# Optimization experiments

Measured on AMD Instinct MI355X. Metric: run time of the kernel, lower is better.

The kernel has to match this reference:

```python
import jax, jax.numpy as jnp
import numpy as np

B, C, H, W = 16, 64, 128, 128


def setup_inputs() -> dict:
    key = jax.random.key(0)
    k1, k2, k3 = jax.random.split(key, 3)
    return {
        "template_map": jax.random.normal(k1, (B, C, H, W), dtype=jnp.float32),
        "roi_map": jax.random.normal(k2, (B, C, H, W), dtype=jnp.float32),
        "gamma": jnp.zeros((1,), dtype=jnp.float32),
        "omega": jnp.zeros((1,), dtype=jnp.float32),
        "conv_w": jax.random.normal(k3, (C, 2 * C), dtype=jnp.float32) * 0.05,
        "conv_b": jnp.zeros((C,), dtype=jnp.float32),
    }


def _chan_attn(x):
    # x: [B, C, H, W] -> attention over channels [B, C, C] and flat values [B, C, N]
    b, c, h, w = x.shape
    v = x.reshape(b, c, h * w)
    energy = jnp.einsum('bcn,bdn->bcd', v, v)  # [B, C, C]
    energy_new = jnp.max(energy, axis=-1, keepdims=True) - energy
    attn = jax.nn.softmax(energy_new, axis=-1)
    return attn, v


def reference(template_map, roi_map, gamma, omega, conv_w, conv_b):
    b, c, th, tw = template_map.shape
    _, _, rh, rw = roi_map.shape
    t_attn, t_v = _chan_attn(template_map)
    r_attn, r_v = _chan_attn(roi_map)
    # cross application: roi attention reweights template channels, and vice versa
    t_out = jnp.einsum('bcd,bdn->bcn', r_attn, t_v).reshape(b, c, th, tw)
    t_out = gamma * t_out + template_map
    r_out = jnp.einsum('bcd,bdn->bcn', t_attn, r_v).reshape(b, c, rh, rw)
    r_out = omega * r_out + roi_map
    fused = jnp.concatenate([t_out, r_out], axis=1)  # [B, 2C, H, W]
    # 1x1 conv == channel-mixing einsum
    out = jnp.einsum('bchw,oc->bohw', fused, conv_w) + conv_b[None, :, None, None]
    return out
```

## Files before the change

### kernel.cpp

```cpp
#include <hip/hip_runtime.h>

typedef __attribute__((ext_vector_type(8))) short short8;
typedef __attribute__((ext_vector_type(4))) float floatx4;
typedef unsigned int uint;
typedef unsigned short ushort;

#define BATCH 16
#define CH 64
#define NPIX 16384
#define TWOC 128
#define XSTR 260

__device__ __forceinline__ ushort f2bf(float f) {
    uint u = __float_as_uint(f);
    u += 0x7FFFu + ((u >> 16) & 1u);
    return (ushort)(u >> 16);
}
__device__ __forceinline__ uint pk2(float lo, float hi) {
    return (uint)f2bf(lo) | ((uint)f2bf(hi) << 16);
}

__global__ __launch_bounds__(256) void gram_kernel(
    const float* __restrict__ tmap, const float* __restrict__ rmap,
    const float* __restrict__ gamma, const float* __restrict__ omega,
    float* __restrict__ G)
{
    const int map = blockIdx.y;
    const float mult = (map == 0) ? omega[0] : gamma[0];
    if (mult == 0.f) return;

    __shared__ float tile[64][68];
    const int chunk = blockIdx.x;
    const int b     = blockIdx.z;
    const float* x = (map == 0 ? tmap : rmap) + (size_t)b * CH * NPIX + chunk * 512;
    const int t  = threadIdx.x;
    const int ti = t >> 4;
    const int tj = t & 15;

    float acc[4][4];
#pragma unroll
    for (int i = 0; i < 4; ++i)
#pragma unroll
        for (int j = 0; j < 4; ++j) acc[i][j] = 0.f;

    for (int tt = 0; tt < 8; ++tt) {
        const int col0 = tt * 64;
#pragma unroll
        for (int k = 0; k < 16; ++k) {
            int e = t + 256 * k;
            int c = e >> 6, col = e & 63;
            tile[c][col] = x[(size_t)c * NPIX + col0 + col];
        }
        __syncthreads();
#pragma unroll 8
        for (int n = 0; n < 64; n += 2) {
            float2 av[4], bv[4];
#pragma unroll
            for (int i = 0; i < 4; ++i) av[i] = *(const float2*)&tile[ti + 16 * i][n];
#pragma unroll
            for (int j = 0; j < 4; ++j) bv[j] = *(const float2*)&tile[tj + 16 * j][n];
#pragma unroll
            for (int i = 0; i < 4; ++i)
#pragma unroll
                for (int j = 0; j < 4; ++j) {
                    acc[i][j] += av[i].x * bv[j].x;
                    acc[i][j] += av[i].y * bv[j].y;
                }
        }
        __syncthreads();
    }
    float* Gp = G + ((size_t)(b * 2 + map) << 12);
#pragma unroll
    for (int i = 0; i < 4; ++i)
#pragma unroll
        for (int j = 0; j < 4; ++j)
            atomicAdd(&Gp[(ti + 16 * i) * 64 + (tj + 16 * j)], acc[i][j]);
}

__global__ __launch_bounds__(128) void finalize_kernel(
    const float* __restrict__ G, const float* __restrict__ gamma,
    const float* __restrict__ omega, const float* __restrict__ conv_w,
    ushort* __restrict__ Mtf)
{
    __shared__ float attn[2][64][64];
    const int b = blockIdx.x;
    const int t = threadIdx.x;
    const float gam = gamma[0], om = omega[0];
    {
        const int map = t >> 6, i = t & 63;
        const float need = (map == 0) ? om : gam;
        if (need != 0.f) {
            const float* Grow = G + ((size_t)(b * 2 + map) << 12) + i * 64;
            float mn = Grow[0];
            for (int j = 1; j < 64; ++j) mn = fminf(mn, Grow[j]);
            float s = 0.f;
            for (int j = 0; j < 64; ++j) s += expf(mn - Grow[j]);
            const float inv = 1.f / s;
            for (int j = 0; j < 64; ++j) attn[map][i][j] = expf(mn - Grow[j]) * inv;
        }
    }
    __syncthreads();
    for (int idx = t; idx < 8192; idx += 128) {
        const int e     = idx & 7;
        const int l     = (idx >> 3) & 63;
        const int mi    = (idx >> 9) & 3;
        const int kstep = idx >> 11;
        const int row = mi * 16 + (l & 15);
        const int k   = kstep * 32 + (l >> 4) * 8 + e;
        const float* wrow = conv_w + row * TWOC;
        float v = wrow[k];
        if (k < 64) {
            if (gam != 0.f) {
                float dot = 0.f;
                for (int c = 0; c < 64; ++c) dot += wrow[c] * attn[1][c][k];
                v += gam * dot;
            }
        } else {
            const int d = k - 64;
            if (om != 0.f) {
                float dot = 0.f;
                for (int c = 0; c < 64; ++c) dot += wrow[64 + c] * attn[0][c][d];
                v += om * dot;
            }
        }
        Mtf[(size_t)b * 8192 + idx] = f2bf(v);
    }
}

__global__ __launch_bounds__(256, 4) void out_kernel(
    const float* __restrict__ tmap, const float* __restrict__ rmap,
    const ushort* __restrict__ Mtf, const float* __restrict__ conv_b,
    float* __restrict__ out)
{
    __shared__ __align__(16) ushort Ms[8192];
    __shared__ __align__(16) uint   Xs[16 * XSTR];

    const int b   = blockIdx.y;
    const int t   = threadIdx.x;
    const int w   = t >> 6;
    const int l   = t & 63;
    const int lg  = l >> 4;
    const int lj  = l & 15;
    const int px0 = blockIdx.x * 256;

    {
        const uint4* src = (const uint4*)(Mtf + (size_t)b * 8192);
        uint4* dst = (uint4*)Ms;
#pragma unroll
        for (int i = 0; i < 4; ++i) dst[t + 256 * i] = src[t + 256 * i];
    }

    floatx4 acc[4][4];
#pragma unroll
    for (int mi = 0; mi < 4; ++mi)
#pragma unroll
        for (int nj = 0; nj < 4; ++nj) acc[mi][nj] = (floatx4){0.f, 0.f, 0.f, 0.f};

    const float* tb = tmap + (size_t)b * CH * NPIX + px0;
    const float* rb = rmap + (size_t)b * CH * NPIX + px0;

#pragma unroll
    for (int c = 0; c < 4; ++c) {
        const float* src = ((c < 2) ? tb : rb) + (size_t)((c & 1) * 32) * NPIX;

        float4 r0[4], r1[4];
#pragma unroll
        for (int it = 0; it < 4; ++it) {
            const int p = it * 4 + w;
            r0[it] = *(const float4*)&src[(size_t)(2 * p) * NPIX + 4 * l];
            r1[it] = *(const float4*)&src[(size_t)(2 * p + 1) * NPIX + 4 * l];
        }
        __syncthreads();

#pragma unroll
        for (int it = 0; it < 4; ++it) {
            const int p = it * 4 + w;
            uint4 o;
            o.x = pk2(r0[it].x, r1[it].x);
            o.y = pk2(r0[it].y, r1[it].y);
            o.z = pk2(r0[it].z, r1[it].z);
            o.w = pk2(r0[it].w, r1[it].w);
            *(uint4*)&Xs[p * XSTR + 4 * l] = o;
        }
        __syncthreads();

        short8 a[4];
#pragma unroll
        for (int mi = 0; mi < 4; ++mi)
            a[mi] = *(const short8*)&Ms[((c * 4 + mi) * 64 + l) * 8];

#pragma unroll
        for (int nj = 0; nj < 4; ++nj) {
            const int pxl = w * 64 + nj * 16 + lj;
            uint4 bu;
            bu.x = Xs[(4 * lg + 0) * XSTR + pxl];
            bu.y = Xs[(4 * lg + 1) * XSTR + pxl];
            bu.z = Xs[(4 * lg + 2) * XSTR + pxl];
            bu.w = Xs[(4 * lg + 3) * XSTR + pxl];
            const short8 bb = *(const short8*)&bu;
#pragma unroll
            for (int mi = 0; mi < 4; ++mi)
                acc[mi][nj] = __builtin_amdgcn_mfma_f32_16x16x32_bf16(
                    a[mi], bb, acc[mi][nj], 0, 0, 0);
        }
    }

    const int pxw = px0 + w * 64;
#pragma unroll
    for (int mi = 0; mi < 4; ++mi) {
#pragma unroll
        for (int r = 0; r < 4; ++r) {
            const int och = mi * 16 + lg * 4 + r;
            const float bv = conv_b[och];
            float* orow = out + ((size_t)b * CH + och) * NPIX;
#pragma unroll
            for (int nj = 0; nj < 4; ++nj)
                orow[pxw + nj * 16 + lj] = acc[mi][nj][r] + bv;
        }
    }
}

extern "C" void kernel_launch(void* const* d_in, const int* in_sizes, int n_in,
                              void* d_out, int out_size, void* d_ws, size_t ws_size,
                              hipStream_t stream) {
    const float* tmap   = (const float*)d_in[0];
    const float* rmap   = (const float*)d_in[1];
    const float* gamma  = (const float*)d_in[2];
    const float* omega  = (const float*)d_in[3];
    const float* conv_w = (const float*)d_in[4];
    const float* conv_b = (const float*)d_in[5];
    float* out = (float*)d_out;

    float*  G   = (float*)d_ws;
    ushort* Mtf = (ushort*)((char*)d_ws + (size_t)BATCH * 2 * 4096 * sizeof(float));

    hipMemsetAsync(d_ws, 0, (size_t)BATCH * 2 * 4096 * sizeof(float), stream);

    gram_kernel<<<dim3(32, 2, BATCH), 256, 0, stream>>>(tmap, rmap, gamma, omega, G);
    finalize_kernel<<<dim3(BATCH), 128, 0, stream>>>(G, gamma, omega, conv_w, Mtf);
    out_kernel<<<dim3(64, BATCH), 256, 0, stream>>>(tmap, rmap, Mtf, conv_b, out);
}
```

Before: 54.46 us.

## Shrink out_kernel to single-wave blocks, drop barriers and LDS weight staging

Restructures the output GEMM kernel so each block is one 64-lane wave handling 64 pixels, with 4x as many blocks. Because a single wave owns its LDS tile, the __syncthreads barriers become an explicit lgkmcnt wait, and the bf16 weight matrix is read straight from global memory/cache instead of being staged in shared memory. This removes barrier stalls and LDS staging overhead and raises the number of independent waves available to hide latency. In exchange, each wave re-reads the weight fragments from global memory, and the smaller per-block pixel span yields shorter 256-byte contiguous row segments per load.

```diff
diff --git a/kernel.cpp b/kernel.cpp
--- a/kernel.cpp
+++ b/kernel.cpp
@@ -9,7 +9,7 @@
 #define CH 64
 #define NPIX 16384
 #define TWOC 128
-#define XSTR 260
+#define XSTR 68
 
 __device__ __forceinline__ ushort f2bf(float f) {
     uint u = __float_as_uint(f);
@@ -127,37 +127,28 @@
     }
 }
 
-__global__ __launch_bounds__(256, 4) void out_kernel(
+__global__ __launch_bounds__(64, 4) void out_kernel(
     const float* __restrict__ tmap, const float* __restrict__ rmap,
     const ushort* __restrict__ Mtf, const float* __restrict__ conv_b,
     float* __restrict__ out)
 {
-    __shared__ __align__(16) ushort Ms[8192];
-    __shared__ __align__(16) uint   Xs[16 * XSTR];
+    __shared__ __align__(16) uint Xs[16 * XSTR];
 
     const int b   = blockIdx.y;
-    const int t   = threadIdx.x;
-    const int w   = t >> 6;
-    const int l   = t & 63;
+    const int l   = threadIdx.x;
     const int lg  = l >> 4;
     const int lj  = l & 15;
-    const int px0 = blockIdx.x * 256;
-
-    {
-        const uint4* src = (const uint4*)(Mtf + (size_t)b * 8192);
-        uint4* dst = (uint4*)Ms;
-#pragma unroll
-        for (int i = 0; i < 4; ++i) dst[t + 256 * i] = src[t + 256 * i];
-    }
+    const int pxw = blockIdx.x * 64;
+
+    const ushort* mbase = Mtf + (size_t)b * 8192;
+    const float*  tb = tmap + (size_t)b * CH * NPIX + pxw;
+    const float*  rb = rmap + (size_t)b * CH * NPIX + pxw;
 
     floatx4 acc[4][4];
 #pragma unroll
     for (int mi = 0; mi < 4; ++mi)
 #pragma unroll
         for (int nj = 0; nj < 4; ++nj) acc[mi][nj] = (floatx4){0.f, 0.f, 0.f, 0.f};
-
-    const float* tb = tmap + (size_t)b * CH * NPIX + px0;
-    const float* rb = rmap + (size_t)b * CH * NPIX + px0;
 
 #pragma unroll
     for (int c = 0; c < 4; ++c) {
@@ -166,37 +157,37 @@
         float4 r0[4], r1[4];
 #pragma unroll
         for (int it = 0; it < 4; ++it) {
-            const int p = it * 4 + w;
-            r0[it] = *(const float4*)&src[(size_t)(2 * p) * NPIX + 4 * l];
-            r1[it] = *(const float4*)&src[(size_t)(2 * p + 1) * NPIX + 4 * l];
-        }
-        __syncthreads();
+            const int p = it * 4 + lg;
+            r0[it] = *(const float4*)&src[(size_t)(2 * p) * NPIX + 4 * lj];
+            r1[it] = *(const float4*)&src[(size_t)(2 * p + 1) * NPIX + 4 * lj];
+        }
 
 #pragma unroll
         for (int it = 0; it < 4; ++it) {
-            const int p = it * 4 + w;
+            const int p = it * 4 + lg;
             uint4 o;
             o.x = pk2(r0[it].x, r1[it].x);
             o.y = pk2(r0[it].y, r1[it].y);
             o.z = pk2(r0[it].z, r1[it].z);
             o.w = pk2(r0[it].w, r1[it].w);
-            *(uint4*)&Xs[p * XSTR + 4 * l] = o;
-        }
-        __syncthreads();
+            *(uint4*)&Xs[p * XSTR + 4 * lj] = o;
+        }
 
         short8 a[4];
 #pragma unroll
         for (int mi = 0; mi < 4; ++mi)
-            a[mi] = *(const short8*)&Ms[((c * 4 + mi) * 64 + l) * 8];
+            a[mi] = *(const short8*)&mbase[((c * 4 + mi) * 64 + l) * 8];
+
+        asm volatile("s_waitcnt lgkmcnt(0)" ::: "memory");
+        __builtin_amdgcn_sched_barrier(0);
 
 #pragma unroll
         for (int nj = 0; nj < 4; ++nj) {
-            const int pxl = w * 64 + nj * 16 + lj;
             uint4 bu;
-            bu.x = Xs[(4 * lg + 0) * XSTR + pxl];
-            bu.y = Xs[(4 * lg + 1) * XSTR + pxl];
-            bu.z = Xs[(4 * lg + 2) * XSTR + pxl];
-            bu.w = Xs[(4 * lg + 3) * XSTR + pxl];
+            bu.x = Xs[(4 * lg + 0) * XSTR + nj * 16 + lj];
+            bu.y = Xs[(4 * lg + 1) * XSTR + nj * 16 + lj];
+            bu.z = Xs[(4 * lg + 2) * XSTR + nj * 16 + lj];
+            bu.w = Xs[(4 * lg + 3) * XSTR + nj * 16 + lj];
             const short8 bb = *(const short8*)&bu;
 #pragma unroll
             for (int mi = 0; mi < 4; ++mi)
@@ -205,7 +196,6 @@
         }
     }
 
-    const int pxw = px0 + w * 64;
 #pragma unroll
     for (int mi = 0; mi < 4; ++mi) {
 #pragma unroll
@@ -238,5 +228,5 @@
 
     gram_kernel<<<dim3(32, 2, BATCH), 256, 0, stream>>>(tmap, rmap, gamma, omega, G);
     finalize_kernel<<<dim3(BATCH), 128, 0, stream>>>(G, gamma, omega, conv_w, Mtf);
-    out_kernel<<<dim3(64, BATCH), 256, 0, stream>>>(tmap, rmap, Mtf, conv_b, out);
-}
+    out_kernel<<<dim3(256, BATCH), 64, 0, stream>>>(tmap, rmap, Mtf, conv_b, out);
+}
```

Result: slower. 58.22 us (+6.9%).
